# Kernel optimization log

Hardware: AMD Instinct MI355X
Metric: run time of the kernel (lower is better)

The kernel has to match this reference:

```python
import jax, jax.numpy as jnp
import numpy as np

B = 4096          # batch_size
D = 256           # embedding dim
N = 2 * B
TEMPERATURE = 0.5
GAMMA = 2.0
ALPHA = 0.25


def _negative_indices():
    # Static column indices of negatives per row: all columns except self (i)
    # and the positive partner ((i+B) mod N). Shape (N, N-2).
    idx = []
    for i in range(N):
        partner = (i + B) % N
        cols = [j for j in range(N) if j != i and j != partner]
        idx.append(cols)
    return np.asarray(idx, dtype=np.int32)

_NEG_IDX = jnp.asarray(_negative_indices())


def setup_inputs() -> dict:
    key = jax.random.key(0)
    kx, ky = jax.random.split(key)
    zx = jax.random.normal(kx, (B, D), dtype=jnp.float32)
    zy = jax.random.normal(ky, (B, D), dtype=jnp.float32)
    return {"zx": zx, "zy": zy}


def reference(zx, zy):
    z = jnp.concatenate([zx, zy], axis=0)                    # (N, D)
    zn = z / jnp.linalg.norm(z, axis=1, keepdims=True)       # cosine normalize
    sim = (zn @ zn.T) / TEMPERATURE                          # (N, N)

    sim_xy = jnp.diagonal(sim, offset=B)                     # (B,)
    sim_yx = jnp.diagonal(sim, offset=-B)                    # (B,)
    pos = jnp.concatenate([sim_xy, sim_yx])[:, None]         # (N, 1)
    neg = jnp.take_along_axis(sim, _NEG_IDX, axis=1)         # (N, N-2)

    logits = jnp.concatenate([pos, neg], axis=1)             # (N, N-1)
    # CE with label 0 for every row: -log_softmax(logits)[:, 0]
    ce = jax.nn.logsumexp(logits, axis=1) - logits[:, 0]
    pt = jnp.exp(-ce)
    focal = (1.0 - pt) ** GAMMA * ce
    return (ALPHA * focal).mean()
```

## Files before the change

### kernel.cpp

```cpp
#include <hip/hip_runtime.h>
#include <stdint.h>
#include <stddef.h>


typedef __attribute__((ext_vector_type(8))) short short8;
typedef __attribute__((ext_vector_type(4))) float f32x4;

#define NROWS 8192
#define DDIM 256

__device__ __forceinline__ unsigned short f2bf(float f) {
  unsigned int u = __float_as_uint(f);
  u = (u + 0x7FFFu + ((u >> 16) & 1u)) >> 16;
  return (unsigned short)u;
}
__device__ __forceinline__ float bf2f(unsigned short s) {
  return __uint_as_float(((unsigned int)s) << 16);
}

__global__ __launch_bounds__(64) void norm_kernel(const float* __restrict__ zx,
                                                  const float* __restrict__ zy,
                                                  unsigned short* __restrict__ zn) {
  const int row = blockIdx.x;
  const int lane = threadIdx.x;
  const float* src = (row < 4096) ? (zx + (size_t)row * DDIM)
                                  : (zy + (size_t)(row - 4096) * DDIM);
  float4 v = reinterpret_cast<const float4*>(src)[lane];
  float ss = v.x * v.x + v.y * v.y + v.z * v.z + v.w * v.w;
#pragma unroll
  for (int m = 1; m < 64; m <<= 1) ss += __shfl_xor(ss, m);
  const float sc = 1.41421356237f * rsqrtf(ss);
  ushort4 o;
  o.x = f2bf(v.x * sc); o.y = f2bf(v.y * sc);
  o.z = f2bf(v.z * sc); o.w = f2bf(v.w * sc);
  reinterpret_cast<ushort4*>(zn + (size_t)row * DDIM)[lane] = o;
}

__global__ __launch_bounds__(64) void pos_kernel(const unsigned short* __restrict__ zn,
                                                 float* __restrict__ pos) {
  const int b = blockIdx.x;
  const int lane = threadIdx.x;
  ushort4 a = reinterpret_cast<const ushort4*>(zn + (size_t)b * DDIM)[lane];
  ushort4 c = reinterpret_cast<const ushort4*>(zn + (size_t)(b + 4096) * DDIM)[lane];
  float s = bf2f(a.x) * bf2f(c.x) + bf2f(a.y) * bf2f(c.y) +
            bf2f(a.z) * bf2f(c.z) + bf2f(a.w) * bf2f(c.w);
#pragma unroll
  for (int m = 1; m < 64; m <<= 1) s += __shfl_xor(s, m);
  if (lane == 0) pos[b] = s;
}

__global__ __launch_bounds__(256, 2) void simexp_kernel(const unsigned short* __restrict__ zn,
                                                        float* __restrict__ partial) {
  __shared__ unsigned short smem[2][2][128 * 64];
  const int bid = blockIdx.x;
  const int panel = bid >> 3;
  const int chunk = bid & 7;
  const int R0 = panel << 7;
  const int tid = threadIdx.x;
  const int lane = tid & 63;
  const int wid = tid >> 6;
  const int wr = wid >> 1;
  const int wc = wid & 1;

  const f32x4 z4 = {0.f, 0.f, 0.f, 0.f};
  f32x4 acc[4][4];
  float rsum[4][4];
#pragma unroll
  for (int m = 0; m < 4; ++m)
#pragma unroll
    for (int n = 0; n < 4; ++n) { acc[m][n] = z4; rsum[m][n] = 0.f; }

  auto stage = [&](int buf, int which, int row0, int k0) {
    unsigned short* lb = &smem[buf][which][0];
#pragma unroll
    for (int j = 0; j < 4; ++j) {
      const int u = j * 256 + wid * 64 + lane;
      const unsigned short* g = zn + (size_t)(row0 + (u >> 3)) * DDIM + k0 + (u & 7) * 8;
      unsigned short* l = lb + (size_t)(j * 256 + wid * 64) * 8;
      __builtin_amdgcn_global_load_lds(
          (const __attribute__((address_space(1))) void*)g,
          (__attribute__((address_space(3))) void*)l, 16, 0, 0);
    }
  };

  stage(0, 0, R0, 0);
  stage(0, 1, chunk * 1024, 0);
  __syncthreads();

  int buf = 0;
  for (int t = 0; t < 8; ++t) {
    for (int kk = 0; kk < 4; ++kk) {
      int nt = t, nkk = kk + 1;
      if (nkk == 4) { nt = t + 1; nkk = 0; }
      if (nt < 8) {
        stage(buf ^ 1, 0, R0, nkk * 64);
        stage(buf ^ 1, 1, chunk * 1024 + nt * 128, nkk * 64);
      }
      const unsigned short* A = &smem[buf][0][0];
      const unsigned short* Bm = &smem[buf][1][0];
#pragma unroll
      for (int ks = 0; ks < 2; ++ks) {
        short8 af[4], bfr[4];
#pragma unroll
        for (int m = 0; m < 4; ++m)
          af[m] = *reinterpret_cast<const short8*>(
              A + ((wr * 64 + m * 16 + (lane & 15)) * 64 + ks * 32 + (lane >> 4) * 8));
#pragma unroll
        for (int n = 0; n < 4; ++n)
          bfr[n] = *reinterpret_cast<const short8*>(
              Bm + ((wc * 64 + n * 16 + (lane & 15)) * 64 + ks * 32 + (lane >> 4) * 8));
#pragma unroll
        for (int m = 0; m < 4; ++m)
#pragma unroll
          for (int n = 0; n < 4; ++n)
            acc[m][n] = __builtin_amdgcn_mfma_f32_16x16x32_bf16(af[m], bfr[n], acc[m][n], 0, 0, 0);
      }
      buf ^= 1;
      __syncthreads();
    }
    const int C0 = chunk * 1024 + t * 128;
#pragma unroll
    for (int m = 0; m < 4; ++m) {
      const int grow_b = R0 + wr * 64 + m * 16 + ((lane >> 4) << 2);
#pragma unroll
      for (int n = 0; n < 4; ++n) {
        const int gcol = C0 + wc * 64 + n * 16 + (lane & 15);
#pragma unroll
        for (int r = 0; r < 4; ++r) {
          const float e = __expf(acc[m][n][r]);
          rsum[m][r] += ((grow_b + r) == gcol) ? 0.f : e;
        }
        acc[m][n] = z4;
      }
    }
  }

#pragma unroll
  for (int m = 0; m < 4; ++m)
#pragma unroll
    for (int r = 0; r < 4; ++r) {
      float s = rsum[m][r];
      s += __shfl_xor(s, 1); s += __shfl_xor(s, 2);
      s += __shfl_xor(s, 4); s += __shfl_xor(s, 8);
      if ((lane & 15) == 0) {
        const int grow = R0 + wr * 64 + m * 16 + ((lane >> 4) << 2) + r;
        partial[(size_t)(chunk * 2 + wc) * NROWS + grow] = s;
      }
    }
}

__global__ __launch_bounds__(256) void d1_kernel(const float* __restrict__ partial,
                                                 const float* __restrict__ pos,
                                                 float* __restrict__ bsum) {
  const int row = blockIdx.x * 256 + threadIdx.x;
  float s = 0.f;
#pragma unroll
  for (int c = 0; c < 16; ++c) s += partial[(size_t)c * NROWS + row];
  const float ce = __logf(s) - pos[row & 4095];
  const float pt = __expf(-ce);
  float f = (1.f - pt) * (1.f - pt) * ce;
#pragma unroll
  for (int m = 1; m < 64; m <<= 1) f += __shfl_xor(f, m);
  __shared__ float wsum[4];
  if ((threadIdx.x & 63) == 0) wsum[threadIdx.x >> 6] = f;
  __syncthreads();
  if (threadIdx.x == 0) bsum[blockIdx.x] = wsum[0] + wsum[1] + wsum[2] + wsum[3];
}

__global__ __launch_bounds__(64) void d2_kernel(const float* __restrict__ bsum,
                                                float* __restrict__ out) {
  const int l = threadIdx.x;
  float v = (l < 32) ? bsum[l] : 0.f;
#pragma unroll
  for (int m = 1; m < 64; m <<= 1) v += __shfl_xor(v, m);
  if (l == 0) out[0] = 0.25f * v / 8192.f;
}

extern "C" void kernel_launch(void* const* d_in, const int* in_sizes, int n_in,
                              void* d_out, int out_size, void* d_ws, size_t ws_size,
                              hipStream_t stream) {
  const float* zx = (const float*)d_in[0];
  const float* zy = (const float*)d_in[1];
  float* out = (float*)d_out;

  unsigned short* zn = (unsigned short*)d_ws;
  float* pos = (float*)((char*)d_ws + (size_t)NROWS * DDIM * 2);
  float* partial = pos + 4096;
  float* bsum = partial + 16 * NROWS;

  norm_kernel<<<NROWS, 64, 0, stream>>>(zx, zy, zn);
  pos_kernel<<<4096, 64, 0, stream>>>(zn, pos);
  simexp_kernel<<<512, 256, 0, stream>>>(zn, partial);
  d1_kernel<<<32, 256, 0, stream>>>(partial, pos, bsum);
  d2_kernel<<<1, 64, 0, stream>>>(bsum, out);
}
```

Before: 111.1 us.

## Exploit symmetry of similarity matrix with upper-triangular tile grid

Since the similarity matrix is symmetric, the kernel now computes only upper-triangular 128x128 tiles (2080 blocks). Each tile contributes its exp sums to both row and column partials, which roughly halves the MFMA and exp work. The positive-pair values are taken from the off-diagonal tiles, so the separate pos kernel is dropped. The norm kernel packs 4 rows per block. In exchange, the partial buffer grows to 128 slices, which makes the reduction kernel read more data. Blocks also do less work each because they no longer loop over 8 column tiles.

```diff
diff --git a/kernel.cpp b/kernel.cpp
--- a/kernel.cpp
+++ b/kernel.cpp
@@ -8,21 +8,19 @@
 
 #define NROWS 8192
 #define DDIM 256
+#define NTILES 2080
 
 __device__ __forceinline__ unsigned short f2bf(float f) {
   unsigned int u = __float_as_uint(f);
   u = (u + 0x7FFFu + ((u >> 16) & 1u)) >> 16;
   return (unsigned short)u;
 }
-__device__ __forceinline__ float bf2f(unsigned short s) {
-  return __uint_as_float(((unsigned int)s) << 16);
-}
-
-__global__ __launch_bounds__(64) void norm_kernel(const float* __restrict__ zx,
-                                                  const float* __restrict__ zy,
-                                                  unsigned short* __restrict__ zn) {
-  const int row = blockIdx.x;
-  const int lane = threadIdx.x;
+
+__global__ __launch_bounds__(256) void norm_kernel(const float* __restrict__ zx,
+                                                   const float* __restrict__ zy,
+                                                   unsigned short* __restrict__ zn) {
+  const int row = blockIdx.x * 4 + (threadIdx.x >> 6);
+  const int lane = threadIdx.x & 63;
   const float* src = (row < 4096) ? (zx + (size_t)row * DDIM)
                                   : (zy + (size_t)(row - 4096) * DDIM);
   float4 v = reinterpret_cast<const float4*>(src)[lane];
@@ -36,26 +34,21 @@
   reinterpret_cast<ushort4*>(zn + (size_t)row * DDIM)[lane] = o;
 }
 
-__global__ __launch_bounds__(64) void pos_kernel(const unsigned short* __restrict__ zn,
-                                                 float* __restrict__ pos) {
-  const int b = blockIdx.x;
-  const int lane = threadIdx.x;
-  ushort4 a = reinterpret_cast<const ushort4*>(zn + (size_t)b * DDIM)[lane];
-  ushort4 c = reinterpret_cast<const ushort4*>(zn + (size_t)(b + 4096) * DDIM)[lane];
-  float s = bf2f(a.x) * bf2f(c.x) + bf2f(a.y) * bf2f(c.y) +
-            bf2f(a.z) * bf2f(c.z) + bf2f(a.w) * bf2f(c.w);
-#pragma unroll
-  for (int m = 1; m < 64; m <<= 1) s += __shfl_xor(s, m);
-  if (lane == 0) pos[b] = s;
-}
-
-__global__ __launch_bounds__(256, 2) void simexp_kernel(const unsigned short* __restrict__ zn,
-                                                        float* __restrict__ partial) {
+__global__ __launch_bounds__(256, 2) void simtri_kernel(const unsigned short* __restrict__ zn,
+                                                        float* __restrict__ partial,
+                                                        float* __restrict__ pos) {
   __shared__ unsigned short smem[2][2][128 * 64];
   const int bid = blockIdx.x;
-  const int panel = bid >> 3;
-  const int chunk = bid & 7;
-  const int R0 = panel << 7;
+  int p = (int)((129.0f - sqrtf((float)(16641 - 8 * bid))) * 0.5f);
+  p = max(0, min(63, p));
+  while ((((p + 1) * (129 - (p + 1))) >> 1) <= bid) ++p;
+  while (((p * (129 - p)) >> 1) > bid) --p;
+  const int q = p + (bid - ((p * (129 - p)) >> 1));
+  const int R0 = p << 7;
+  const int C0 = q << 7;
+  const bool isdiag = (p == q);
+  const bool ispos = (q == p + 32);
+
   const int tid = threadIdx.x;
   const int lane = tid & 63;
   const int wid = tid >> 6;
@@ -64,11 +57,10 @@
 
   const f32x4 z4 = {0.f, 0.f, 0.f, 0.f};
   f32x4 acc[4][4];
-  float rsum[4][4];
 #pragma unroll
   for (int m = 0; m < 4; ++m)
 #pragma unroll
-    for (int n = 0; n < 4; ++n) { acc[m][n] = z4; rsum[m][n] = 0.f; }
+    for (int n = 0; n < 4; ++n) acc[m][n] = z4;
 
   auto stage = [&](int buf, int which, int row0, int k0) {
     unsigned short* lb = &smem[buf][which][0];
@@ -84,53 +76,62 @@
   };
 
   stage(0, 0, R0, 0);
-  stage(0, 1, chunk * 1024, 0);
+  if (!isdiag) stage(0, 1, C0, 0);
   __syncthreads();
 
   int buf = 0;
-  for (int t = 0; t < 8; ++t) {
-    for (int kk = 0; kk < 4; ++kk) {
-      int nt = t, nkk = kk + 1;
-      if (nkk == 4) { nt = t + 1; nkk = 0; }
-      if (nt < 8) {
-        stage(buf ^ 1, 0, R0, nkk * 64);
-        stage(buf ^ 1, 1, chunk * 1024 + nt * 128, nkk * 64);
-      }
-      const unsigned short* A = &smem[buf][0][0];
-      const unsigned short* Bm = &smem[buf][1][0];
-#pragma unroll
-      for (int ks = 0; ks < 2; ++ks) {
-        short8 af[4], bfr[4];
-#pragma unroll
-        for (int m = 0; m < 4; ++m)
-          af[m] = *reinterpret_cast<const short8*>(
-              A + ((wr * 64 + m * 16 + (lane & 15)) * 64 + ks * 32 + (lane >> 4) * 8));
+#pragma unroll
+  for (int s = 0; s < 4; ++s) {
+    if (s < 3) {
+      stage(buf ^ 1, 0, R0, (s + 1) * 64);
+      if (!isdiag) stage(buf ^ 1, 1, C0, (s + 1) * 64);
+    }
+    const unsigned short* A = &smem[buf][0][0];
+    const unsigned short* Bm = isdiag ? A : &smem[buf][1][0];
+#pragma unroll
+    for (int ks = 0; ks < 2; ++ks) {
+      short8 af[4], bfr[4];
+#pragma unroll
+      for (int m = 0; m < 4; ++m)
+        af[m] = *reinterpret_cast<const short8*>(
+            A + ((wr * 64 + m * 16 + (lane & 15)) * 64 + ks * 32 + (lane >> 4) * 8));
+#pragma unroll
+      for (int n = 0; n < 4; ++n)
+        bfr[n] = *reinterpret_cast<const short8*>(
+            Bm + ((wc * 64 + n * 16 + (lane & 15)) * 64 + ks * 32 + (lane >> 4) * 8));
+#pragma unroll
+      for (int m = 0; m < 4; ++m)
 #pragma unroll
         for (int n = 0; n < 4; ++n)
-          bfr[n] = *reinterpret_cast<const short8*>(
-              Bm + ((wc * 64 + n * 16 + (lane & 15)) * 64 + ks * 32 + (lane >> 4) * 8));
-#pragma unroll
-        for (int m = 0; m < 4; ++m)
-#pragma unroll
-          for (int n = 0; n < 4; ++n)
-            acc[m][n] = __builtin_amdgcn_mfma_f32_16x16x32_bf16(af[m], bfr[n], acc[m][n], 0, 0, 0);
-      }
-      buf ^= 1;
-      __syncthreads();
-    }
-    const int C0 = chunk * 1024 + t * 128;
-#pragma unroll
-    for (int m = 0; m < 4; ++m) {
-      const int grow_b = R0 + wr * 64 + m * 16 + ((lane >> 4) << 2);
-#pragma unroll
-      for (int n = 0; n < 4; ++n) {
-        const int gcol = C0 + wc * 64 + n * 16 + (lane & 15);
-#pragma unroll
-        for (int r = 0; r < 4; ++r) {
-          const float e = __expf(acc[m][n][r]);
-          rsum[m][r] += ((grow_b + r) == gcol) ? 0.f : e;
-        }
-        acc[m][n] = z4;
+          acc[m][n] = __builtin_amdgcn_mfma_f32_16x16x32_bf16(af[m], bfr[n], acc[m][n], 0, 0, 0);
+    }
+    buf ^= 1;
+    __syncthreads();
+  }
+
+  float rsum[4][4];
+  float csum[4];
+#pragma unroll
+  for (int m = 0; m < 4; ++m)
+#pragma unroll
+    for (int r = 0; r < 4; ++r) rsum[m][r] = 0.f;
+#pragma unroll
+  for (int n = 0; n < 4; ++n) csum[n] = 0.f;
+
+#pragma unroll
+  for (int m = 0; m < 4; ++m) {
+    const int grow_b = R0 + wr * 64 + m * 16 + ((lane >> 4) << 2);
+#pragma unroll
+    for (int n = 0; n < 4; ++n) {
+      const int gcol = C0 + wc * 64 + n * 16 + (lane & 15);
+#pragma unroll
+      for (int r = 0; r < 4; ++r) {
+        const int grow = grow_b + r;
+        const float val = acc[m][n][r];
+        if (ispos && (gcol == grow + 4096)) pos[grow] = val;
+        const float e = (isdiag && (grow == gcol)) ? 0.f : __expf(val);
+        rsum[m][r] += e;
+        csum[n] += e;
       }
     }
   }
@@ -144,9 +145,19 @@
       s += __shfl_xor(s, 4); s += __shfl_xor(s, 8);
       if ((lane & 15) == 0) {
         const int grow = R0 + wr * 64 + m * 16 + ((lane >> 4) << 2) + r;
-        partial[(size_t)(chunk * 2 + wc) * NROWS + grow] = s;
+        partial[(size_t)(q * 2 + wc) * NROWS + grow] = s;
       }
     }
+
+  if (!isdiag) {
+#pragma unroll
+    for (int n = 0; n < 4; ++n) {
+      float c = csum[n];
+      c += __shfl_xor(c, 16); c += __shfl_xor(c, 32);
+      if (lane < 16)
+        partial[(size_t)(p * 2 + wr) * NROWS + (C0 + wc * 64 + n * 16 + lane)] = c;
+    }
+  }
 }
 
 __global__ __launch_bounds__(256) void d1_kernel(const float* __restrict__ partial,
@@ -154,8 +165,8 @@
                                                  float* __restrict__ bsum) {
   const int row = blockIdx.x * 256 + threadIdx.x;
   float s = 0.f;
-#pragma unroll
-  for (int c = 0; c < 16; ++c) s += partial[(size_t)c * NROWS + row];
+#pragma unroll 16
+  for (int c = 0; c < 128; ++c) s += partial[(size_t)c * NROWS + row];
   const float ce = __logf(s) - pos[row & 4095];
   const float pt = __expf(-ce);
   float f = (1.f - pt) * (1.f - pt) * ce;
@@ -186,11 +197,10 @@
   unsigned short* zn = (unsigned short*)d_ws;
   float* pos = (float*)((char*)d_ws + (size_t)NROWS * DDIM * 2);
   float* partial = pos + 4096;
-  float* bsum = partial + 16 * NROWS;
-
-  norm_kernel<<<NROWS, 64, 0, stream>>>(zx, zy, zn);
-  pos_kernel<<<4096, 64, 0, stream>>>(zn, pos);
-  simexp_kernel<<<512, 256, 0, stream>>>(zn, partial);
+  float* bsum = partial + (size_t)128 * NROWS;
+
+  norm_kernel<<<2048, 256, 0, stream>>>(zx, zy, zn);
+  simtri_kernel<<<NTILES, 256, 0, stream>>>(zn, partial, pos);
   d1_kernel<<<32, 256, 0, stream>>>(partial, pos, bsum);
   d2_kernel<<<1, 64, 0, stream>>>(bsum, out);
 }
```

Result: no change. 112.6 us (+1.3%).
